# Kernel optimization log

Measured on AMD Instinct MI355X. Metric: run time of the kernel, lower is better.

The kernel has to match this reference:

```python
import jax, jax.numpy as jnp
import numpy as np

DIM = 768
HEADS = 12
SCALE = DIM ** -0.5  # NOTE: module scales by full dim, not head dim


def setup_inputs() -> dict:
    key = jax.random.key(0)
    ks = jax.random.split(key, 5)
    B, N, C = 8, 1024, DIM
    x = jax.random.normal(ks[0], (B, N, C), dtype=jnp.float32)
    W_qkv = jax.random.normal(ks[1], (C, 3 * C), dtype=jnp.float32) * (C ** -0.5)
    b_qkv = jnp.zeros((3 * C,), dtype=jnp.float32)
    W_out = jax.random.normal(ks[2], (C, C), dtype=jnp.float32) * (C ** -0.5)
    b_out = jnp.zeros((C,), dtype=jnp.float32)
    return {"x": x, "W_qkv": W_qkv, "b_qkv": b_qkv, "W_out": W_out, "b_out": b_out}


def reference(x, W_qkv, b_qkv, W_out, b_out) -> jnp.ndarray:
    B, N, C = x.shape
    H, D = HEADS, C // HEADS
    qkv = x @ W_qkv + b_qkv                       # [B, N, 3C]
    q, k, v = jnp.split(qkv, 3, axis=-1)
    # [B, N, C] -> [B, H, N, D]
    q = q.reshape(B, N, H, D).transpose(0, 2, 1, 3)
    k = k.reshape(B, N, H, D).transpose(0, 2, 1, 3)
    v = v.reshape(B, N, H, D).transpose(0, 2, 1, 3)
    attn = jnp.einsum("bhnd,bhmd->bhnm", q, k) * SCALE
    attn = jax.nn.softmax(attn, axis=-1)
    out = jnp.einsum("bhnm,bhmd->bhnd", attn, v)   # [B, H, N, D]
    out = out.transpose(0, 2, 1, 3).reshape(B, N, C)
    return out @ W_out + b_out
```

## Files before the change

### kernel.cpp

```cpp
#include <hip/hip_runtime.h>
#include <hip/hip_bf16.h>

typedef __attribute__((ext_vector_type(4))) float f32x4;
typedef __attribute__((ext_vector_type(4))) unsigned u32x4;
typedef __attribute__((ext_vector_type(8))) short bf16x8;

#define SCALE_F 0.03608439182435161f
#define QSCALE  (0.03608439182435161f * 1.44269504088896f)

__device__ __forceinline__ unsigned short f2bf(float f) {
    union { float f; unsigned u; } v; v.f = f;
    return (unsigned short)((v.u + 0x7FFFu + ((v.u >> 16) & 1u)) >> 16);
}

__device__ __forceinline__ float fast_exp2(float x) {
#if __has_builtin(__builtin_amdgcn_exp2f)
    return __builtin_amdgcn_exp2f(x);
#else
    return exp2f(x);
#endif
}

__device__ __forceinline__ void gload_lds16(const void* g, void* l) {
    __builtin_amdgcn_global_load_lds(
        (const __attribute__((address_space(1))) unsigned int*)g,
        (__attribute__((address_space(3))) unsigned int*)l, 16, 0, 0);
}

__global__ __launch_bounds__(256) void xcvt_kernel(const float* __restrict__ X,
                                                   unsigned short* __restrict__ Xb,
                                                   int n8) {
    const int i = blockIdx.x * 256 + threadIdx.x;
    if (i < n8) {
        f32x4 a = *(const f32x4*)(X + (size_t)i * 8);
        f32x4 b = *(const f32x4*)(X + (size_t)i * 8 + 4);
        bf16x8 w;
#pragma unroll
        for (int j = 0; j < 4; ++j) { w[j] = (short)f2bf(a[j]); w[4 + j] = (short)f2bf(b[j]); }
        *(bf16x8*)(Xb + (size_t)i * 8) = w;
    }
}

__global__ __launch_bounds__(256) void wtrans_kernel(const float* __restrict__ W,
                                                     unsigned short* __restrict__ WT,
                                                     int R, int C) {
    __shared__ unsigned short T[64][68];
    const int t = threadIdx.x;
    const int r0 = blockIdx.y * 64, c0 = blockIdx.x * 64;
    {
        const int lr = t >> 4, lc = (t & 15) * 4;
#pragma unroll
        for (int p = 0; p < 4; ++p) {
            const float* s = W + (size_t)(r0 + lr + p * 16) * C + c0 + lc;
            f32x4 v = *(const f32x4*)s;
            unsigned short* d = &T[lr + p * 16][lc];
            d[0] = f2bf(v[0]); d[1] = f2bf(v[1]); d[2] = f2bf(v[2]); d[3] = f2bf(v[3]);
        }
    }
    __syncthreads();
    {
        const int oc = t >> 3, j0 = (t & 7) * 8;
#pragma unroll
        for (int p = 0; p < 2; ++p) {
            const int c = oc + p * 32;
            bf16x8 v;
#pragma unroll
            for (int j = 0; j < 8; ++j) v[j] = (short)T[j0 + j][c];
            *(bf16x8*)(WT + (size_t)(c0 + c) * R + r0 + j0) = v;
        }
    }
}

__global__ __launch_bounds__(256) void qkv_gemm_kernel(
    const unsigned short* __restrict__ Xb, const unsigned short* __restrict__ WT,
    const float* __restrict__ bias,
    unsigned short* __restrict__ Qw, unsigned short* __restrict__ Kw,
    unsigned short* __restrict__ VTw)
{
    __shared__ unsigned short Alds[128 * 32];
    __shared__ unsigned short Blds[128 * 32];

    const int t = threadIdx.x;
    const int lane = t & 63, wave = t >> 6;
    const int l15 = lane & 15, l4 = lane >> 4;
    const int m0 = blockIdx.x * 128, n0 = blockIdx.y * 128;
    const int wr = wave >> 1, wc = wave & 1;

    f32x4 acc[4][4];
#pragma unroll
    for (int m = 0; m < 4; ++m)
#pragma unroll
        for (int n = 0; n < 4; ++n) acc[m][n] = (f32x4){0.f, 0.f, 0.f, 0.f};

    for (int k0 = 0; k0 < 768; k0 += 32) {
#pragma unroll
        for (int c = 0; c < 2; ++c) {
            const int o = wave * 1024 + lane * 16 + c * 4096;
            const int row = o >> 6, cb = o & 63;
            gload_lds16((const char*)(Xb + (size_t)(m0 + row) * 768 + k0) + cb,
                        (char*)Alds + wave * 1024 + c * 4096);
            gload_lds16((const char*)(WT + (size_t)(n0 + row) * 768 + k0) + cb,
                        (char*)Blds + wave * 1024 + c * 4096);
        }
        __syncthreads();
        bf16x8 af[4], bfr[4];
#pragma unroll
        for (int m = 0; m < 4; ++m)
            af[m] = *(const bf16x8*)((const char*)Alds + (wr * 64 + m * 16 + l15) * 64 + l4 * 16);
#pragma unroll
        for (int n = 0; n < 4; ++n)
            bfr[n] = *(const bf16x8*)((const char*)Blds + (wc * 64 + n * 16 + l15) * 64 + l4 * 16);
#pragma unroll
        for (int m = 0; m < 4; ++m)
#pragma unroll
            for (int n = 0; n < 4; ++n)
                acc[m][n] = __builtin_amdgcn_mfma_f32_16x16x32_bf16(af[m], bfr[n], acc[m][n], 0, 0, 0);
        __syncthreads();
    }

#pragma unroll
    for (int n = 0; n < 4; ++n) {
        const int col = n0 + wc * 64 + n * 16 + l15;
        const float bv = bias[col];
        const int which = col / 768;
        const int cc = col - which * 768;
        const int h = cc >> 6, dd = cc & 63;
#pragma unroll
        for (int m = 0; m < 4; ++m) {
#pragma unroll
            for (int r = 0; r < 4; ++r) {
                const int row = m0 + wr * 64 + m * 16 + l4 * 4 + r;
                const int b = row >> 10, ntok = row & 1023;
                const size_t bh = (size_t)b * 12 + h;
                float val = acc[m][n][r] + bv;
                if (which == 0) val *= QSCALE;
                const unsigned short hv = f2bf(val);
                if (which == 0)      Qw[(bh * 1024 + ntok) * 64 + dd] = hv;
                else if (which == 1) Kw[(bh * 1024 + ntok) * 64 + dd] = hv;
                else                 VTw[(bh * 64 + dd) * 1024 + ntok] = hv;
            }
        }
    }
}

__global__ __launch_bounds__(256) void attn_kernel(
    const unsigned short* __restrict__ Qw, const unsigned short* __restrict__ Kw,
    const unsigned short* __restrict__ VTw, unsigned short* __restrict__ A2)
{
    __shared__ unsigned short Klds[2 * 64 * 64];
    __shared__ unsigned short Vlds[2 * 64 * 64];
    __shared__ float Flds[4 * 16];

    const int t = threadIdx.x, lane = t & 63, wave = t >> 6;
    const int l15 = lane & 15, l4 = lane >> 4;
    const int wg = (blockIdx.x & 7) * 192 + (blockIdx.x >> 3);
    const int qt = wg & 15, bh = wg >> 4;
    const int q0 = qt * 64;

    const size_t kvbase = (size_t)bh * 1024 * 64;
    const size_t vtbase = (size_t)bh * 64 * 1024;

    const unsigned short* qptr = Qw + kvbase + (size_t)(q0 + wave * 16 + l15) * 64;
    const bf16x8 qf0 = *(const bf16x8*)((const char*)qptr + l4 * 16);
    const bf16x8 qf1 = *(const bf16x8*)((const char*)qptr + 64 + l4 * 16);

    f32x4 oacc[4];
#pragma unroll
    for (int d = 0; d < 4; ++d) oacc[d] = (f32x4){0.f, 0.f, 0.f, 0.f};
    float m_run = -1e30f, l_run = 0.f;

    auto STAGE = [&](int kt, int bufi) {
        const int kv0 = kt * 64;
        char* kb = (char*)Klds + bufi * 8192;
        char* vb = (char*)Vlds + bufi * 8192;
#pragma unroll
        for (int c = 0; c < 2; ++c) {
            const int oo = wave * 1024 + lane * 16 + c * 4096;
            const int R = oo >> 7, w = oo & 127;
            const int sw = w ^ ((R & 7) << 4);
            const int kvs = (R & 0x23) | ((R & 0x0C) << 1) | ((R & 0x10) >> 2);
            gload_lds16((const char*)(Kw + kvbase + (size_t)(kv0 + kvs) * 64) + sw,
                        kb + wave * 1024 + c * 4096);
            gload_lds16((const char*)(VTw + vtbase + (size_t)R * 1024 + kv0) + sw,
                        vb + wave * 1024 + c * 4096);
        }
    };

    STAGE(0, 0);
    for (int kt = 0; kt < 16; ++kt) {
        const int cur = kt & 1;
        if (kt < 15) {
            STAGE(kt + 1, cur ^ 1);
            asm volatile("s_waitcnt vmcnt(4)" ::: "memory");
        } else {
            asm volatile("s_waitcnt vmcnt(0)" ::: "memory");
        }
        __builtin_amdgcn_s_barrier();
        __builtin_amdgcn_sched_barrier(0);
        const char* kb = (const char*)Klds + cur * 8192;
        const char* vb = (const char*)Vlds + cur * 8192;

        f32x4 sacc[4];
#pragma unroll
        for (int i = 0; i < 4; ++i) sacc[i] = (f32x4){0.f, 0.f, 0.f, 0.f};
        __builtin_amdgcn_s_setprio(1);
#pragma unroll
        for (int ks = 0; ks < 2; ++ks) {
            const bf16x8 qq = ks ? qf1 : qf0;
#pragma unroll
            for (int kvf = 0; kvf < 4; ++kvf) {
                const int row = kvf * 16 + l15;
                int addr = row * 128 + ks * 64 + l4 * 16;
                addr ^= (row & 7) << 4;
                const bf16x8 kf = *(const bf16x8*)(kb + addr);
                sacc[kvf] = __builtin_amdgcn_mfma_f32_16x16x32_bf16(kf, qq, sacc[kvf], 0, 0, 0);
            }
        }
        __builtin_amdgcn_s_setprio(0);

        float p[16];
        float tmax = -1e30f;
#pragma unroll
        for (int i = 0; i < 4; ++i)
#pragma unroll
            for (int r = 0; r < 4; ++r) {
                p[i * 4 + r] = sacc[i][r];
                tmax = fmaxf(tmax, sacc[i][r]);
            }
        tmax = fmaxf(tmax, __shfl_xor(tmax, 16));
        tmax = fmaxf(tmax, __shfl_xor(tmax, 32));

        if (!__all(tmax - m_run <= 8.f)) {
            const float mnew = fmaxf(m_run, tmax);
            const float alpha = fast_exp2(m_run - mnew);
            m_run = mnew;
            if (lane < 16) Flds[wave * 16 + lane] = alpha;
            const f32x4 av = *(const f32x4*)(&Flds[wave * 16 + l4 * 4]);
#pragma unroll
            for (int d = 0; d < 4; ++d)
#pragma unroll
                for (int r = 0; r < 4; ++r) oacc[d][r] *= av[r];
            l_run *= alpha;
        }

        float tsum = 0.f;
#pragma unroll
        for (int i = 0; i < 16; ++i) { p[i] = fast_exp2(p[i] - m_run); tsum += p[i]; }
        tsum += __shfl_xor(tsum, 16);
        tsum += __shfl_xor(tsum, 32);
        l_run += tsum;

        bf16x8 paf[2];
#pragma unroll
        for (int ks = 0; ks < 2; ++ks) {
            union { u32x4 u; bf16x8 h; } cv;
#pragma unroll
            for (int j2 = 0; j2 < 4; ++j2)
                asm("v_cvt_pk_bf16_f32 %0, %1, %2"
                    : "=v"(cv.u[j2]) : "v"(p[ks * 8 + 2 * j2]), "v"(p[ks * 8 + 2 * j2 + 1]));
            paf[ks] = cv.h;
        }

        __builtin_amdgcn_s_setprio(1);
#pragma unroll
        for (int ks = 0; ks < 2; ++ks) {
#pragma unroll
            for (int df = 0; df < 4; ++df) {
                const int d = df * 16 + l15;
                int addr = d * 128 + ks * 64 + l4 * 16;
                addr ^= (d & 7) << 4;
                const bf16x8 vf = *(const bf16x8*)(vb + addr);
                oacc[df] = __builtin_amdgcn_mfma_f32_16x16x32_bf16(paf[ks], vf, oacc[df], 0, 0, 0);
            }
        }
        __builtin_amdgcn_s_setprio(0);
        __builtin_amdgcn_s_barrier();
    }

    if (lane < 16) Flds[wave * 16 + lane] = 1.f / l_run;
    const f32x4 inv = *(const f32x4*)(&Flds[wave * 16 + l4 * 4]);
    const int b = bh / 12, h = bh - b * 12;
#pragma unroll
    for (int df = 0; df < 4; ++df) {
#pragma unroll
        for (int r = 0; r < 4; ++r) {
            const int row = b * 1024 + q0 + wave * 16 + l4 * 4 + r;
            const int col = h * 64 + df * 16 + l15;
            A2[(size_t)row * 768 + col] = f2bf(oacc[df][r] * inv[r]);
        }
    }
}

__global__ __launch_bounds__(256) void out_gemm_kernel(
    const unsigned short* __restrict__ A2, const unsigned short* __restrict__ WT,
    const float* __restrict__ bias, float* __restrict__ Out)
{
    __shared__ unsigned short Alds[128 * 32];
    __shared__ unsigned short Blds[64 * 32];

    const int t = threadIdx.x;
    const int lane = t & 63, wave = t >> 6;
    const int l15 = lane & 15, l4 = lane >> 4;
    const int m0 = blockIdx.x * 128, n0 = blockIdx.y * 64;
    const int wr = wave >> 1, wc = wave & 1;

    f32x4 acc[4][2];
#pragma unroll
    for (int m = 0; m < 4; ++m)
#pragma unroll
        for (int n = 0; n < 2; ++n) acc[m][n] = (f32x4){0.f, 0.f, 0.f, 0.f};

    for (int k0 = 0; k0 < 768; k0 += 32) {
#pragma unroll
        for (int c = 0; c < 2; ++c) {
            const int o = wave * 1024 + lane * 16 + c * 4096;
            const int row = o >> 6, cb = o & 63;
            gload_lds16((const char*)(A2 + (size_t)(m0 + row) * 768 + k0) + cb,
                        (char*)Alds + wave * 1024 + c * 4096);
        }
        {
            const int o = t * 16;
            const int row = o >> 6, cb = o & 63;
            gload_lds16((const char*)(WT + (size_t)(n0 + row) * 768 + k0) + cb,
                        (char*)Blds + o);
        }
        __syncthreads();
        bf16x8 af[4], bfr[2];
#pragma unroll
        for (int m = 0; m < 4; ++m)
            af[m] = *(const bf16x8*)((const char*)Alds + (wr * 64 + m * 16 + l15) * 64 + l4 * 16);
#pragma unroll
        for (int n = 0; n < 2; ++n)
            bfr[n] = *(const bf16x8*)((const char*)Blds + (wc * 32 + n * 16 + l15) * 64 + l4 * 16);
#pragma unroll
        for (int m = 0; m < 4; ++m)
#pragma unroll
            for (int n = 0; n < 2; ++n)
                acc[m][n] = __builtin_amdgcn_mfma_f32_16x16x32_bf16(af[m], bfr[n], acc[m][n], 0, 0, 0);
        __syncthreads();
    }

#pragma unroll
    for (int n = 0; n < 2; ++n) {
        const int col = n0 + wc * 32 + n * 16 + l15;
        const float bv = bias[col];
#pragma unroll
        for (int m = 0; m < 4; ++m)
#pragma unroll
            for (int r = 0; r < 4; ++r) {
                const int row = m0 + wr * 64 + m * 16 + l4 * 4 + r;
                Out[(size_t)row * 768 + col] = acc[m][n][r] + bv;
            }
    }
}

extern "C" void kernel_launch(void* const* d_in, const int* in_sizes, int n_in,
                              void* d_out, int out_size, void* d_ws, size_t ws_size,
                              hipStream_t stream) {
    const float* X    = (const float*)d_in[0];
    const float* Wqkv = (const float*)d_in[1];
    const float* bqkv = (const float*)d_in[2];
    const float* Wout = (const float*)d_in[3];
    const float* bout = (const float*)d_in[4];
    float* Out = (float*)d_out;

    const size_t nq = (size_t)96 * 1024 * 64;
    unsigned short* XbA2  = (unsigned short*)d_ws;
    unsigned short* Qw    = XbA2 + nq;
    unsigned short* Kw    = Qw + nq;
    unsigned short* VTw   = Kw + nq;
    unsigned short* WqkvT = VTw + nq;
    unsigned short* WoutT = WqkvT + (size_t)2304 * 768;

    hipLaunchKernelGGL(xcvt_kernel, dim3(3072), dim3(256), 0, stream,
                       X, XbA2, 8192 * 768 / 8);
    hipLaunchKernelGGL(wtrans_kernel, dim3(36, 12), dim3(256), 0, stream,
                       Wqkv, WqkvT, 768, 2304);
    hipLaunchKernelGGL(wtrans_kernel, dim3(12, 12), dim3(256), 0, stream,
                       Wout, WoutT, 768, 768);
    hipLaunchKernelGGL(qkv_gemm_kernel, dim3(64, 18), dim3(256), 0, stream,
                       XbA2, WqkvT, bqkv, Qw, Kw, VTw);
    hipLaunchKernelGGL(attn_kernel, dim3(1536), dim3(256), 0, stream,
                       Qw, Kw, VTw, XbA2);
    hipLaunchKernelGGL(out_gemm_kernel, dim3(64, 12), dim3(256), 0, stream,
                       XbA2, WoutT, bout, Out);
}
```

Before: 137.7 us.

## Double-buffer LDS in QKV and output GEMMs; restructure attention loop barriers

Both projection GEMMs now keep two LDS buffers and issue the next K-slice's global-to-LDS loads before computing on the current slice, with one wait-and-barrier per iteration instead of two __syncthreads. MFMA sections are raised in priority with setprio. The attention loop drops its partial vmcnt(4) wait at the top and instead waits on all loads at the end of each iteration. This is meant to overlap memory latency with MFMA work, at the cost of more LDS per block and possibly lower occupancy. The attention reorder removes the barrier between the end of one iteration's reads and the next prefetch; that looks safe only because the end-of-iteration barrier remains.

```diff
diff --git a/kernel.cpp b/kernel.cpp
--- a/kernel.cpp
+++ b/kernel.cpp
@@ -77,8 +77,8 @@
     unsigned short* __restrict__ Qw, unsigned short* __restrict__ Kw,
     unsigned short* __restrict__ VTw)
 {
-    __shared__ unsigned short Alds[128 * 32];
-    __shared__ unsigned short Blds[128 * 32];
+    __shared__ unsigned short Alds[2][128 * 32];
+    __shared__ unsigned short Blds[2][128 * 32];
 
     const int t = threadIdx.x;
     const int lane = t & 63, wave = t >> 6;
@@ -92,30 +92,45 @@
 #pragma unroll
         for (int n = 0; n < 4; ++n) acc[m][n] = (f32x4){0.f, 0.f, 0.f, 0.f};
 
-    for (int k0 = 0; k0 < 768; k0 += 32) {
+    auto STAGE = [&](int k0, int bufi) {
 #pragma unroll
         for (int c = 0; c < 2; ++c) {
             const int o = wave * 1024 + lane * 16 + c * 4096;
             const int row = o >> 6, cb = o & 63;
             gload_lds16((const char*)(Xb + (size_t)(m0 + row) * 768 + k0) + cb,
-                        (char*)Alds + wave * 1024 + c * 4096);
+                        (char*)&Alds[bufi][0] + wave * 1024 + c * 4096);
             gload_lds16((const char*)(WT + (size_t)(n0 + row) * 768 + k0) + cb,
-                        (char*)Blds + wave * 1024 + c * 4096);
-        }
-        __syncthreads();
+                        (char*)&Blds[bufi][0] + wave * 1024 + c * 4096);
+        }
+    };
+
+    STAGE(0, 0);
+    asm volatile("s_waitcnt vmcnt(0)" ::: "memory");
+    __builtin_amdgcn_s_barrier();
+
+    for (int kt = 0; kt < 24; ++kt) {
+        const int cur = kt & 1;
+        if (kt < 23) STAGE((kt + 1) * 32, cur ^ 1);
+
         bf16x8 af[4], bfr[4];
 #pragma unroll
         for (int m = 0; m < 4; ++m)
-            af[m] = *(const bf16x8*)((const char*)Alds + (wr * 64 + m * 16 + l15) * 64 + l4 * 16);
+            af[m] = *(const bf16x8*)((const char*)&Alds[cur][0] + (wr * 64 + m * 16 + l15) * 64 + l4 * 16);
 #pragma unroll
         for (int n = 0; n < 4; ++n)
-            bfr[n] = *(const bf16x8*)((const char*)Blds + (wc * 64 + n * 16 + l15) * 64 + l4 * 16);
+            bfr[n] = *(const bf16x8*)((const char*)&Blds[cur][0] + (wc * 64 + n * 16 + l15) * 64 + l4 * 16);
+        __builtin_amdgcn_s_setprio(1);
 #pragma unroll
         for (int m = 0; m < 4; ++m)
 #pragma unroll
             for (int n = 0; n < 4; ++n)
                 acc[m][n] = __builtin_amdgcn_mfma_f32_16x16x32_bf16(af[m], bfr[n], acc[m][n], 0, 0, 0);
-        __syncthreads();
+        __builtin_amdgcn_s_setprio(0);
+
+        if (kt < 23) {
+            asm volatile("s_waitcnt vmcnt(0)" ::: "memory");
+            __builtin_amdgcn_s_barrier();
+        }
     }
 
 #pragma unroll
@@ -187,16 +202,12 @@
     };
 
     STAGE(0, 0);
+    asm volatile("s_waitcnt vmcnt(0)" ::: "memory");
+    __builtin_amdgcn_s_barrier();
+
     for (int kt = 0; kt < 16; ++kt) {
         const int cur = kt & 1;
-        if (kt < 15) {
-            STAGE(kt + 1, cur ^ 1);
-            asm volatile("s_waitcnt vmcnt(4)" ::: "memory");
-        } else {
-            asm volatile("s_waitcnt vmcnt(0)" ::: "memory");
-        }
-        __builtin_amdgcn_s_barrier();
-        __builtin_amdgcn_sched_barrier(0);
+        if (kt < 15) STAGE(kt + 1, cur ^ 1);
         const char* kb = (const char*)Klds + cur * 8192;
         const char* vb = (const char*)Vlds + cur * 8192;
 
@@ -274,7 +285,11 @@
             }
         }
         __builtin_amdgcn_s_setprio(0);
-        __builtin_amdgcn_s_barrier();
+
+        if (kt < 15) {
+            asm volatile("s_waitcnt vmcnt(0)" ::: "memory");
+            __builtin_amdgcn_s_barrier();
+        }
     }
 
     if (lane < 16) Flds[wave * 16 + lane] = 1.f / l_run;
@@ -295,8 +310,8 @@
     const unsigned short* __restrict__ A2, const unsigned short* __restrict__ WT,
     const float* __restrict__ bias, float* __restrict__ Out)
 {
-    __shared__ unsigned short Alds[128 * 32];
-    __shared__ unsigned short Blds[64 * 32];
+    __shared__ unsigned short Alds[2][128 * 32];
+    __shared__ unsigned short Blds[2][64 * 32];
 
     const int t = threadIdx.x;
     const int lane = t & 63, wave = t >> 6;
@@ -310,34 +325,49 @@
 #pragma unroll
         for (int n = 0; n < 2; ++n) acc[m][n] = (f32x4){0.f, 0.f, 0.f, 0.f};
 
-    for (int k0 = 0; k0 < 768; k0 += 32) {
+    auto STAGE = [&](int k0, int bufi) {
 #pragma unroll
         for (int c = 0; c < 2; ++c) {
             const int o = wave * 1024 + lane * 16 + c * 4096;
             const int row = o >> 6, cb = o & 63;
             gload_lds16((const char*)(A2 + (size_t)(m0 + row) * 768 + k0) + cb,
-                        (char*)Alds + wave * 1024 + c * 4096);
+                        (char*)&Alds[bufi][0] + wave * 1024 + c * 4096);
         }
         {
             const int o = t * 16;
             const int row = o >> 6, cb = o & 63;
             gload_lds16((const char*)(WT + (size_t)(n0 + row) * 768 + k0) + cb,
-                        (char*)Blds + o);
-        }
-        __syncthreads();
+                        (char*)&Blds[bufi][0] + o);
+        }
+    };
+
+    STAGE(0, 0);
+    asm volatile("s_waitcnt vmcnt(0)" ::: "memory");
+    __builtin_amdgcn_s_barrier();
+
+    for (int kt = 0; kt < 24; ++kt) {
+        const int cur = kt & 1;
+        if (kt < 23) STAGE((kt + 1) * 32, cur ^ 1);
+
         bf16x8 af[4], bfr[2];
 #pragma unroll
         for (int m = 0; m < 4; ++m)
-            af[m] = *(const bf16x8*)((const char*)Alds + (wr * 64 + m * 16 + l15) * 64 + l4 * 16);
+            af[m] = *(const bf16x8*)((const char*)&Alds[cur][0] + (wr * 64 + m * 16 + l15) * 64 + l4 * 16);
 #pragma unroll
         for (int n = 0; n < 2; ++n)
-            bfr[n] = *(const bf16x8*)((const char*)Blds + (wc * 32 + n * 16 + l15) * 64 + l4 * 16);
+            bfr[n] = *(const bf16x8*)((const char*)&Blds[cur][0] + (wc * 32 + n * 16 + l15) * 64 + l4 * 16);
+        __builtin_amdgcn_s_setprio(1);
 #pragma unroll
         for (int m = 0; m < 4; ++m)
 #pragma unroll
             for (int n = 0; n < 2; ++n)
                 acc[m][n] = __builtin_amdgcn_mfma_f32_16x16x32_bf16(af[m], bfr[n], acc[m][n], 0, 0, 0);
-        __syncthreads();
+        __builtin_amdgcn_s_setprio(0);
+
+        if (kt < 23) {
+            asm volatile("s_waitcnt vmcnt(0)" ::: "memory");
+            __builtin_amdgcn_s_barrier();
+        }
     }
 
 #pragma unroll
```

Result: no change. 140.4 us (+2.0%).

## Double QKV GEMM K-tile to 64 with XOR-swizzled LDS and MFMA priority

Applied to the files above, without the earlier changes.

The QKV projection GEMM now stages a 64-wide K slice per iteration instead of 32, which halves the number of barrier pairs and load rounds. The global-to-LDS copies and the fragment reads use an XOR swizzle on the row index to avoid LDS bank conflicts with the wider 128-byte rows. The MFMA loop is wrapped in s_setprio to favour the math waves. LDS use per block doubles, which may reduce occupancy.

```diff
diff --git a/kernel.cpp b/kernel.cpp
--- a/kernel.cpp
+++ b/kernel.cpp
@@ -77,8 +77,8 @@
     unsigned short* __restrict__ Qw, unsigned short* __restrict__ Kw,
     unsigned short* __restrict__ VTw)
 {
-    __shared__ unsigned short Alds[128 * 32];
-    __shared__ unsigned short Blds[128 * 32];
+    __shared__ unsigned short Alds[128 * 64];
+    __shared__ unsigned short Blds[128 * 64];
 
     const int t = threadIdx.x;
     const int lane = t & 63, wave = t >> 6;
@@ -92,29 +92,45 @@
 #pragma unroll
         for (int n = 0; n < 4; ++n) acc[m][n] = (f32x4){0.f, 0.f, 0.f, 0.f};
 
-    for (int k0 = 0; k0 < 768; k0 += 32) {
-#pragma unroll
-        for (int c = 0; c < 2; ++c) {
-            const int o = wave * 1024 + lane * 16 + c * 4096;
-            const int row = o >> 6, cb = o & 63;
-            gload_lds16((const char*)(Xb + (size_t)(m0 + row) * 768 + k0) + cb,
-                        (char*)Alds + wave * 1024 + c * 4096);
-            gload_lds16((const char*)(WT + (size_t)(n0 + row) * 768 + k0) + cb,
-                        (char*)Blds + wave * 1024 + c * 4096);
+    for (int k0 = 0; k0 < 768; k0 += 64) {
+#pragma unroll
+        for (int c = 0; c < 4; ++c) {
+            const int base = wave * 4096 + c * 1024;
+            const int oo = base + lane * 16;
+            const int R = oo >> 7, w = oo & 127;
+            const int sw = w ^ ((R & 7) << 4);
+            gload_lds16((const char*)(Xb + (size_t)(m0 + R) * 768 + k0) + sw,
+                        (char*)Alds + base);
+            gload_lds16((const char*)(WT + (size_t)(n0 + R) * 768 + k0) + sw,
+                        (char*)Blds + base);
         }
         __syncthreads();
-        bf16x8 af[4], bfr[4];
-#pragma unroll
-        for (int m = 0; m < 4; ++m)
-            af[m] = *(const bf16x8*)((const char*)Alds + (wr * 64 + m * 16 + l15) * 64 + l4 * 16);
-#pragma unroll
-        for (int n = 0; n < 4; ++n)
-            bfr[n] = *(const bf16x8*)((const char*)Blds + (wc * 64 + n * 16 + l15) * 64 + l4 * 16);
-#pragma unroll
-        for (int m = 0; m < 4; ++m)
-#pragma unroll
-            for (int n = 0; n < 4; ++n)
-                acc[m][n] = __builtin_amdgcn_mfma_f32_16x16x32_bf16(af[m], bfr[n], acc[m][n], 0, 0, 0);
+
+        bf16x8 af[2][4], bfr[2][4];
+#pragma unroll
+        for (int ks = 0; ks < 2; ++ks) {
+#pragma unroll
+            for (int m = 0; m < 4; ++m) {
+                const int row = wr * 64 + m * 16 + l15;
+                const int ba = (row * 128 + ks * 64 + l4 * 16) ^ ((row & 7) << 4);
+                af[ks][m] = *(const bf16x8*)((const char*)Alds + ba);
+            }
+#pragma unroll
+            for (int n = 0; n < 4; ++n) {
+                const int row = wc * 64 + n * 16 + l15;
+                const int ba = (row * 128 + ks * 64 + l4 * 16) ^ ((row & 7) << 4);
+                bfr[ks][n] = *(const bf16x8*)((const char*)Blds + ba);
+            }
+        }
+        __builtin_amdgcn_s_setprio(1);
+#pragma unroll
+        for (int ks = 0; ks < 2; ++ks)
+#pragma unroll
+            for (int m = 0; m < 4; ++m)
+#pragma unroll
+                for (int n = 0; n < 4; ++n)
+                    acc[m][n] = __builtin_amdgcn_mfma_f32_16x16x32_bf16(af[ks][m], bfr[ks][n], acc[m][n], 0, 0, 0);
+        __builtin_amdgcn_s_setprio(0);
         __syncthreads();
     }
 
```

Result: no change. 139.0 us (+0.9%).
